# Performance work log

Measured on AMD Instinct MI355X. Metric: run time of the kernel, lower is better.

Reference implementation:

```python
import jax, jax.numpy as jnp
import numpy as np

EPS = 1e-5
D = 16
N = 4194304
P_DROP = 0.1


def setup_inputs() -> dict:
    key = jax.random.key(0)
    ks = jax.random.split(key, 4)
    x = jax.random.normal(ks[0], (N, D), dtype=jnp.float32)
    # Learned parameters (LayerNorm default init: weight=1, bias=0; Linear: U(-1/sqrt(d), 1/sqrt(d)))
    bound = 1.0 / np.sqrt(D)
    fc_w = jax.random.uniform(ks[1], (D, D), dtype=jnp.float32, minval=-bound, maxval=bound)
    fc_b = jax.random.uniform(ks[2], (D,), dtype=jnp.float32, minval=-bound, maxval=bound)
    ln1_w = jnp.ones((D,), jnp.float32)
    ln1_b = jnp.zeros((D,), jnp.float32)
    ln2_w = jnp.ones((D,), jnp.float32)
    ln2_b = jnp.zeros((D,), jnp.float32)
    # Dropout realized as a fixed pre-sampled inverted mask (keep_prob scaling baked in),
    # matching torch.nn.Dropout(p=0.1) in training mode for one concrete RNG draw.
    keep = (jax.random.uniform(ks[3], (N, D)) >= P_DROP).astype(jnp.float32)
    drop_mask = keep / (1.0 - P_DROP)
    return {"x": x, "ln1_w": ln1_w, "ln1_b": ln1_b, "fc_w": fc_w, "fc_b": fc_b,
            "ln2_w": ln2_w, "ln2_b": ln2_b, "drop_mask": drop_mask}


def _layernorm(h, w, b):
    mu = jnp.mean(h, axis=-1, keepdims=True)
    var = jnp.mean(jnp.square(h - mu), axis=-1, keepdims=True)  # biased var, like torch LN
    return (h - mu) * jax.lax.rsqrt(var + EPS) * w + b


def reference(x, ln1_w, ln1_b, fc_w, fc_b, ln2_w, ln2_b, drop_mask):
    h = _layernorm(x, ln1_w, ln1_b)            # [N, D]
    h = h @ fc_w.T + fc_b                      # Linear(d, d)
    h = jax.nn.relu(h * drop_mask)             # Dropout (inverted mask) -> ReLU
    return _layernorm(h, ln2_w, ln2_b)         # [N, D]
```

## Files before the change

kernel.cpp:

```cpp
#include <hip/hip_runtime.h>

#define DD 16
#define EPS 1e-5f
#define BLOCK 256
#define GRID 1024

typedef float floatx4 __attribute__((ext_vector_type(4)));

__global__ __launch_bounds__(BLOCK) void twoln_kernel(
    const float* __restrict__ x,
    const float* __restrict__ ln1w, const float* __restrict__ ln1b,
    const float* __restrict__ fcw,  const float* __restrict__ fcb,
    const float* __restrict__ ln2w, const float* __restrict__ ln2b,
    const float* __restrict__ mask,
    float* __restrict__ out, long long nrows)
{
    const int lane = threadIdx.x & 63;
    const int p    = lane & 3;
    const int rsub = lane >> 2;

    float l1w[4], l1b[4], l2w[4], l2b[4], fb[4];
#pragma unroll
    for (int kk = 0; kk < 4; ++kk) {
        l1w[kk] = ln1w[4 * p + kk];
        l1b[kk] = ln1b[4 * p + kk];
        l2w[kk] = ln2w[4 * p + kk];
        l2b[kk] = ln2b[4 * p + kk];
    }
#pragma unroll
    for (int jj = 0; jj < 4; ++jj) fb[jj] = fcb[4 * p + jj];

    float Wreg[4][4][4];
#pragma unroll
    for (int jj = 0; jj < 4; ++jj) {
#pragma unroll
        for (int c = 0; c < 4; ++c) {
            const float4 wv = *reinterpret_cast<const float4*>(
                fcw + (4 * p + jj) * DD + 4 * (p ^ c));
            Wreg[jj][c][0] = wv.x; Wreg[jj][c][1] = wv.y;
            Wreg[jj][c][2] = wv.z; Wreg[jj][c][3] = wv.w;
        }
    }

    const long long ngroups = (nrows + 15) >> 4;
    const long long gw0 = (long long)blockIdx.x * (BLOCK / 64) + (threadIdx.x >> 6);
    const long long nw  = (long long)gridDim.x * (BLOCK / 64);

    const float4* __restrict__ xf = reinterpret_cast<const float4*>(x);
    const float4* __restrict__ mf = reinterpret_cast<const float4*>(mask);
    floatx4* __restrict__ of = reinterpret_cast<floatx4*>(out);

    for (long long g = gw0; g < ngroups; g += nw) {
        const long long row = g * 16 + rsub;
        const bool act = row < nrows;
        const long long idx = g * 64 + lane;

        float4 xv = act ? xf[idx] : make_float4(0.f, 0.f, 0.f, 0.f);
        float4 mv = act ? mf[idx] : make_float4(0.f, 0.f, 0.f, 0.f);

        float sl = xv.x + xv.y + xv.z + xv.w;
        sl += __shfl_xor(sl, 1);
        sl += __shfl_xor(sl, 2);
        const float mu1 = sl * (1.0f / DD);

        const float e0 = xv.x - mu1, e1 = xv.y - mu1, e2 = xv.z - mu1, e3 = xv.w - mu1;
        float vl = e0 * e0 + e1 * e1 + e2 * e2 + e3 * e3;
        vl += __shfl_xor(vl, 1);
        vl += __shfl_xor(vl, 2);
        const float rs1 = rsqrtf(vl * (1.0f / DD) + EPS);

        float h[4];
        h[0] = e0 * rs1 * l1w[0] + l1b[0];
        h[1] = e1 * rs1 * l1w[1] + l1b[1];
        h[2] = e2 * rs1 * l1w[2] + l1b[2];
        h[3] = e3 * rs1 * l1w[3] + l1b[3];

        float ch[4][4];
#pragma unroll
        for (int kk = 0; kk < 4; ++kk) ch[0][kk] = h[kk];
#pragma unroll
        for (int kk = 0; kk < 4; ++kk) ch[1][kk] = __shfl_xor(h[kk], 1);
#pragma unroll
        for (int kk = 0; kk < 4; ++kk) ch[2][kk] = __shfl_xor(h[kk], 2);
#pragma unroll
        for (int kk = 0; kk < 4; ++kk) ch[3][kk] = __shfl_xor(ch[1][kk], 2);

        float gv[4];
#pragma unroll
        for (int jj = 0; jj < 4; ++jj) {
            float acc = fb[jj];
#pragma unroll
            for (int c = 0; c < 4; ++c)
#pragma unroll
                for (int kk = 0; kk < 4; ++kk)
                    acc = fmaf(ch[c][kk], Wreg[jj][c][kk], acc);
            gv[jj] = acc;
        }
        gv[0] = fmaxf(gv[0] * mv.x, 0.f);
        gv[1] = fmaxf(gv[1] * mv.y, 0.f);
        gv[2] = fmaxf(gv[2] * mv.z, 0.f);
        gv[3] = fmaxf(gv[3] * mv.w, 0.f);

        float s2 = gv[0] + gv[1] + gv[2] + gv[3];
        s2 += __shfl_xor(s2, 1);
        s2 += __shfl_xor(s2, 2);
        const float mu2 = s2 * (1.0f / DD);

        const float d0 = gv[0] - mu2, d1 = gv[1] - mu2, d2 = gv[2] - mu2, d3 = gv[3] - mu2;
        float v2 = d0 * d0 + d1 * d1 + d2 * d2 + d3 * d3;
        v2 += __shfl_xor(v2, 1);
        v2 += __shfl_xor(v2, 2);
        const float rs2 = rsqrtf(v2 * (1.0f / DD) + EPS);

        floatx4 ov;
        ov.x = d0 * rs2 * l2w[0] + l2b[0];
        ov.y = d1 * rs2 * l2w[1] + l2b[1];
        ov.z = d2 * rs2 * l2w[2] + l2b[2];
        ov.w = d3 * rs2 * l2w[3] + l2b[3];

        if (act) __builtin_nontemporal_store(ov, &of[idx]);
    }
}

extern "C" void kernel_launch(void* const* d_in, const int* in_sizes, int n_in,
                              void* d_out, int out_size, void* d_ws, size_t ws_size,
                              hipStream_t stream)
{
    const float* x     = (const float*)d_in[0];
    const float* ln1w  = (const float*)d_in[1];
    const float* ln1b  = (const float*)d_in[2];
    const float* fcw   = (const float*)d_in[3];
    const float* fcb   = (const float*)d_in[4];
    const float* ln2w  = (const float*)d_in[5];
    const float* ln2b  = (const float*)d_in[6];
    const float* mask  = (const float*)d_in[7];
    float* out = (float*)d_out;

    const long long nrows = (long long)in_sizes[0] / DD;
    twoln_kernel<<<GRID, BLOCK, 0, stream>>>(x, ln1w, ln1b, fcw, fcb,
                                             ln2w, ln2b, mask, out, nrows);
}
```

Baseline: 151.8 us.

## Add exact-fit specialized kernel with register prefetch and larger grid

Doubles the grid size. Adds a templated fast path for the case where rows divide evenly across warps. That path drops the bounds checks and prefetches the next iteration's x and mask into registers so loads overlap compute, and it reads the mask with nontemporal loads. The intent is to hide memory latency in this bandwidth-bound kernel, at the cost of extra live registers.

```diff
diff --git a/kernel.cpp b/kernel.cpp
--- a/kernel.cpp
+++ b/kernel.cpp
@@ -3,10 +3,11 @@
 #define DD 16
 #define EPS 1e-5f
 #define BLOCK 256
-#define GRID 1024
+#define GRID 2048
 
 typedef float floatx4 __attribute__((ext_vector_type(4)));
 
+template<bool EXACT>
 __global__ __launch_bounds__(BLOCK) void twoln_kernel(
     const float* __restrict__ x,
     const float* __restrict__ ln1w, const float* __restrict__ ln1b,
@@ -46,79 +47,156 @@
     const long long gw0 = (long long)blockIdx.x * (BLOCK / 64) + (threadIdx.x >> 6);
     const long long nw  = (long long)gridDim.x * (BLOCK / 64);
 
-    const float4* __restrict__ xf = reinterpret_cast<const float4*>(x);
-    const float4* __restrict__ mf = reinterpret_cast<const float4*>(mask);
+    const floatx4* __restrict__ xf = reinterpret_cast<const floatx4*>(x);
+    const floatx4* __restrict__ mf = reinterpret_cast<const floatx4*>(mask);
     floatx4* __restrict__ of = reinterpret_cast<floatx4*>(out);
 
-    for (long long g = gw0; g < ngroups; g += nw) {
-        const long long row = g * 16 + rsub;
-        const bool act = row < nrows;
-        const long long idx = g * 64 + lane;
-
-        float4 xv = act ? xf[idx] : make_float4(0.f, 0.f, 0.f, 0.f);
-        float4 mv = act ? mf[idx] : make_float4(0.f, 0.f, 0.f, 0.f);
-
-        float sl = xv.x + xv.y + xv.z + xv.w;
-        sl += __shfl_xor(sl, 1);
-        sl += __shfl_xor(sl, 2);
-        const float mu1 = sl * (1.0f / DD);
-
-        const float e0 = xv.x - mu1, e1 = xv.y - mu1, e2 = xv.z - mu1, e3 = xv.w - mu1;
-        float vl = e0 * e0 + e1 * e1 + e2 * e2 + e3 * e3;
-        vl += __shfl_xor(vl, 1);
-        vl += __shfl_xor(vl, 2);
-        const float rs1 = rsqrtf(vl * (1.0f / DD) + EPS);
-
-        float h[4];
-        h[0] = e0 * rs1 * l1w[0] + l1b[0];
-        h[1] = e1 * rs1 * l1w[1] + l1b[1];
-        h[2] = e2 * rs1 * l1w[2] + l1b[2];
-        h[3] = e3 * rs1 * l1w[3] + l1b[3];
-
-        float ch[4][4];
-#pragma unroll
-        for (int kk = 0; kk < 4; ++kk) ch[0][kk] = h[kk];
-#pragma unroll
-        for (int kk = 0; kk < 4; ++kk) ch[1][kk] = __shfl_xor(h[kk], 1);
-#pragma unroll
-        for (int kk = 0; kk < 4; ++kk) ch[2][kk] = __shfl_xor(h[kk], 2);
-#pragma unroll
-        for (int kk = 0; kk < 4; ++kk) ch[3][kk] = __shfl_xor(ch[1][kk], 2);
-
-        float gv[4];
-#pragma unroll
-        for (int jj = 0; jj < 4; ++jj) {
-            float acc = fb[jj];
-#pragma unroll
-            for (int c = 0; c < 4; ++c)
-#pragma unroll
-                for (int kk = 0; kk < 4; ++kk)
-                    acc = fmaf(ch[c][kk], Wreg[jj][c][kk], acc);
-            gv[jj] = acc;
+    if (EXACT) {
+        if (gw0 >= ngroups) return;
+        floatx4 xv_n = xf[gw0 * 64 + lane];
+        floatx4 mv_n = __builtin_nontemporal_load(&mf[gw0 * 64 + lane]);
+
+        for (long long g = gw0; g < ngroups; g += nw) {
+            const floatx4 xv = xv_n;
+            const floatx4 mv = mv_n;
+            const long long gn = g + nw;
+            if (gn < ngroups) {
+                xv_n = xf[gn * 64 + lane];
+                mv_n = __builtin_nontemporal_load(&mf[gn * 64 + lane]);
+            }
+
+            float sl = xv[0] + xv[1] + xv[2] + xv[3];
+            sl += __shfl_xor(sl, 1);
+            sl += __shfl_xor(sl, 2);
+            const float mu1 = sl * (1.0f / DD);
+            const float e0 = xv[0] - mu1, e1 = xv[1] - mu1,
+                        e2 = xv[2] - mu1, e3 = xv[3] - mu1;
+            float vl = e0 * e0 + e1 * e1 + e2 * e2 + e3 * e3;
+            vl += __shfl_xor(vl, 1);
+            vl += __shfl_xor(vl, 2);
+            const float rs1 = rsqrtf(vl * (1.0f / DD) + EPS);
+
+            float h[4];
+            h[0] = e0 * rs1 * l1w[0] + l1b[0];
+            h[1] = e1 * rs1 * l1w[1] + l1b[1];
+            h[2] = e2 * rs1 * l1w[2] + l1b[2];
+            h[3] = e3 * rs1 * l1w[3] + l1b[3];
+
+            float ch[4][4];
+#pragma unroll
+            for (int kk = 0; kk < 4; ++kk) ch[0][kk] = h[kk];
+#pragma unroll
+            for (int kk = 0; kk < 4; ++kk) ch[1][kk] = __shfl_xor(h[kk], 1);
+#pragma unroll
+            for (int kk = 0; kk < 4; ++kk) ch[2][kk] = __shfl_xor(h[kk], 2);
+#pragma unroll
+            for (int kk = 0; kk < 4; ++kk) ch[3][kk] = __shfl_xor(ch[1][kk], 2);
+
+            float gv[4];
+#pragma unroll
+            for (int jj = 0; jj < 4; ++jj) {
+                float acc = fb[jj];
+#pragma unroll
+                for (int c = 0; c < 4; ++c)
+#pragma unroll
+                    for (int kk = 0; kk < 4; ++kk)
+                        acc = fmaf(ch[c][kk], Wreg[jj][c][kk], acc);
+                gv[jj] = acc;
+            }
+            gv[0] = fmaxf(gv[0] * mv[0], 0.f);
+            gv[1] = fmaxf(gv[1] * mv[1], 0.f);
+            gv[2] = fmaxf(gv[2] * mv[2], 0.f);
+            gv[3] = fmaxf(gv[3] * mv[3], 0.f);
+
+            float s2 = gv[0] + gv[1] + gv[2] + gv[3];
+            s2 += __shfl_xor(s2, 1);
+            s2 += __shfl_xor(s2, 2);
+            const float mu2 = s2 * (1.0f / DD);
+            const float d0 = gv[0] - mu2, d1 = gv[1] - mu2,
+                        d2 = gv[2] - mu2, d3 = gv[3] - mu2;
+            float v2 = d0 * d0 + d1 * d1 + d2 * d2 + d3 * d3;
+            v2 += __shfl_xor(v2, 1);
+            v2 += __shfl_xor(v2, 2);
+            const float rs2 = rsqrtf(v2 * (1.0f / DD) + EPS);
+
+            floatx4 ov;
+            ov[0] = d0 * rs2 * l2w[0] + l2b[0];
+            ov[1] = d1 * rs2 * l2w[1] + l2b[1];
+            ov[2] = d2 * rs2 * l2w[2] + l2b[2];
+            ov[3] = d3 * rs2 * l2w[3] + l2b[3];
+
+            __builtin_nontemporal_store(ov, &of[g * 64 + lane]);
         }
-        gv[0] = fmaxf(gv[0] * mv.x, 0.f);
-        gv[1] = fmaxf(gv[1] * mv.y, 0.f);
-        gv[2] = fmaxf(gv[2] * mv.z, 0.f);
-        gv[3] = fmaxf(gv[3] * mv.w, 0.f);
-
-        float s2 = gv[0] + gv[1] + gv[2] + gv[3];
-        s2 += __shfl_xor(s2, 1);
-        s2 += __shfl_xor(s2, 2);
-        const float mu2 = s2 * (1.0f / DD);
-
-        const float d0 = gv[0] - mu2, d1 = gv[1] - mu2, d2 = gv[2] - mu2, d3 = gv[3] - mu2;
-        float v2 = d0 * d0 + d1 * d1 + d2 * d2 + d3 * d3;
-        v2 += __shfl_xor(v2, 1);
-        v2 += __shfl_xor(v2, 2);
-        const float rs2 = rsqrtf(v2 * (1.0f / DD) + EPS);
-
-        floatx4 ov;
-        ov.x = d0 * rs2 * l2w[0] + l2b[0];
-        ov.y = d1 * rs2 * l2w[1] + l2b[1];
-        ov.z = d2 * rs2 * l2w[2] + l2b[2];
-        ov.w = d3 * rs2 * l2w[3] + l2b[3];
-
-        if (act) __builtin_nontemporal_store(ov, &of[idx]);
+    } else {
+        for (long long g = gw0; g < ngroups; g += nw) {
+            const long long row = g * 16 + rsub;
+            const bool act = row < nrows;
+            const long long idx = g * 64 + lane;
+            floatx4 xv = {0.f, 0.f, 0.f, 0.f}, mv = {0.f, 0.f, 0.f, 0.f};
+            if (act) { xv = xf[idx]; mv = mf[idx]; }
+
+            float sl = xv[0] + xv[1] + xv[2] + xv[3];
+            sl += __shfl_xor(sl, 1);
+            sl += __shfl_xor(sl, 2);
+            const float mu1 = sl * (1.0f / DD);
+            const float e0 = xv[0] - mu1, e1 = xv[1] - mu1,
+                        e2 = xv[2] - mu1, e3 = xv[3] - mu1;
+            float vl = e0 * e0 + e1 * e1 + e2 * e2 + e3 * e3;
+            vl += __shfl_xor(vl, 1);
+            vl += __shfl_xor(vl, 2);
+            const float rs1 = rsqrtf(vl * (1.0f / DD) + EPS);
+
+            float h[4];
+            h[0] = e0 * rs1 * l1w[0] + l1b[0];
+            h[1] = e1 * rs1 * l1w[1] + l1b[1];
+            h[2] = e2 * rs1 * l1w[2] + l1b[2];
+            h[3] = e3 * rs1 * l1w[3] + l1b[3];
+
+            float ch[4][4];
+#pragma unroll
+            for (int kk = 0; kk < 4; ++kk) ch[0][kk] = h[kk];
+#pragma unroll
+            for (int kk = 0; kk < 4; ++kk) ch[1][kk] = __shfl_xor(h[kk], 1);
+#pragma unroll
+            for (int kk = 0; kk < 4; ++kk) ch[2][kk] = __shfl_xor(h[kk], 2);
+#pragma unroll
+            for (int kk = 0; kk < 4; ++kk) ch[3][kk] = __shfl_xor(ch[1][kk], 2);
+
+            float gv[4];
+#pragma unroll
+            for (int jj = 0; jj < 4; ++jj) {
+                float acc = fb[jj];
+#pragma unroll
+                for (int c = 0; c < 4; ++c)
+#pragma unroll
+                    for (int kk = 0; kk < 4; ++kk)
+                        acc = fmaf(ch[c][kk], Wreg[jj][c][kk], acc);
+                gv[jj] = acc;
+            }
+            gv[0] = fmaxf(gv[0] * mv[0], 0.f);
+            gv[1] = fmaxf(gv[1] * mv[1], 0.f);
+            gv[2] = fmaxf(gv[2] * mv[2], 0.f);
+            gv[3] = fmaxf(gv[3] * mv[3], 0.f);
+
+            float s2 = gv[0] + gv[1] + gv[2] + gv[3];
+            s2 += __shfl_xor(s2, 1);
+            s2 += __shfl_xor(s2, 2);
+            const float mu2 = s2 * (1.0f / DD);
+            const float d0 = gv[0] - mu2, d1 = gv[1] - mu2,
+                        d2 = gv[2] - mu2, d3 = gv[3] - mu2;
+            float v2 = d0 * d0 + d1 * d1 + d2 * d2 + d3 * d3;
+            v2 += __shfl_xor(v2, 1);
+            v2 += __shfl_xor(v2, 2);
+            const float rs2 = rsqrtf(v2 * (1.0f / DD) + EPS);
+
+            floatx4 ov;
+            ov[0] = d0 * rs2 * l2w[0] + l2b[0];
+            ov[1] = d1 * rs2 * l2w[1] + l2b[1];
+            ov[2] = d2 * rs2 * l2w[2] + l2b[2];
+            ov[3] = d3 * rs2 * l2w[3] + l2b[3];
+
+            if (act) __builtin_nontemporal_store(ov, &of[idx]);
+        }
     }
 }
 
@@ -137,6 +215,14 @@
     float* out = (float*)d_out;
 
     const long long nrows = (long long)in_sizes[0] / DD;
-    twoln_kernel<<<GRID, BLOCK, 0, stream>>>(x, ln1w, ln1b, fcw, fcb,
-                                             ln2w, ln2b, mask, out, nrows);
+    const long long ngroups = (nrows + 15) >> 4;
+    const long long nw = (long long)GRID * (BLOCK / 64);
+    const bool exact = (nrows % 16 == 0) && (ngroups % nw == 0);
+
+    if (exact)
+        twoln_kernel<true><<<GRID, BLOCK, 0, stream>>>(
+            x, ln1w, ln1b, fcw, fcb, ln2w, ln2b, mask, out, nrows);
+    else
+        twoln_kernel<false><<<GRID, BLOCK, 0, stream>>>(
+            x, ln1w, ln1b, fcw, fcb, ln2w, ln2b, mask, out, nrows);
 }
```

Measured after the change: 122.2 us. 1.24x faster.
